# Optimization experiments

Hardware: AMD Instinct MI355X
Metric: run time of the kernel (lower is better)

The kernel has to match this reference:

```python
import jax, jax.numpy as jnp
import numpy as np

N = 50000      # nodes
E = 800000     # message-passing edges
EF = 1000000   # decoder (full) edges
IN = 128       # in_channels
H = 64         # hidden_channels
OUT = 1        # out_channels
T = 128        # num_timesteps
RESCALE = 4000.0  # SinusoidalPosEmb rescale_steps


def sinusoidal_pos_emb(t, dim, num_steps):
    # t: [N] int -> [N, dim]
    x = t.astype(jnp.float32) * (RESCALE / num_steps)
    half = dim // 2
    freqs = jnp.exp(jnp.arange(half, dtype=jnp.float32) * (-jnp.log(10000.0) / (half - 1)))
    ang = x[:, None] * freqs[None, :]            # [N, half]
    return jnp.concatenate([jnp.sin(ang), jnp.cos(ang)], axis=-1)


def gcn_conv(h, W, b, row, col, norm, n):
    # standard GCNConv: linear -> gather src -> scale by sym norm -> scatter-add to dst -> +bias
    x = h @ W                                     # [N, H]
    msg = x[row] * norm[:, None]                  # [E+N, H]
    out = jax.ops.segment_sum(msg, col, num_segments=n)
    return out + b


def setup_inputs() -> dict:
    key = jax.random.key(0)
    ks = jax.random.split(key, 12)
    rn = lambda k, shape, s=0.02: jax.random.normal(k, shape, jnp.float32) * s
    return {
        "x": jax.random.normal(ks[0], (N, IN), jnp.float32),
        "edge_index": jax.random.randint(ks[1], (2, E), 0, N, jnp.int32),
        "full_edge_index": jax.random.randint(ks[2], (2, EF), 0, N, jnp.int32),
        "time_steps": jax.random.randint(ks[3], (N,), 0, T, jnp.int32),
        "W_in": rn(ks[4], (IN, H)), "b_in": jnp.zeros((H,), jnp.float32),
        "W_t1": rn(ks[5], (H, 4 * H)), "b_t1": jnp.zeros((4 * H,), jnp.float32),
        "W_t2": rn(ks[6], (4 * H, H)), "b_t2": jnp.zeros((H,), jnp.float32),
        "W_c0": rn(ks[7], (H, H)), "b_c0": jnp.zeros((H,), jnp.float32),
        "W_c1": rn(ks[8], (H, H)), "b_c1": jnp.zeros((H,), jnp.float32),
        "W_d1": rn(ks[9], (2 * H, H)), "b_d1": jnp.zeros((H,), jnp.float32),
        "W_d2": rn(ks[10], (H, OUT)), "b_d2": jnp.zeros((OUT,), jnp.float32),
    }


def reference(x, edge_index, full_edge_index, time_steps,
              W_in, b_in, W_t1, b_t1, W_t2, b_t2,
              W_c0, b_c0, W_c1, b_c1, W_d1, b_d1, W_d2, b_d2):
    n = x.shape[0]
    # --- embedder (dropout is identity in eval mode) ---
    h = x @ W_in + b_in                                        # [N, H]
    pe = sinusoidal_pos_emb(time_steps, H, T)                  # [N, H]
    t_emb = jax.nn.silu(pe @ W_t1 + b_t1) @ W_t2 + b_t2        # [N, H]
    h_embed = h + t_emb

    # --- GCN encoder: add self-loops once, symmetric normalization ---
    loops = jnp.arange(n, dtype=edge_index.dtype)
    row = jnp.concatenate([edge_index[0], loops])              # [E+N]
    col = jnp.concatenate([edge_index[1], loops])
    deg = jax.ops.segment_sum(jnp.ones_like(col, jnp.float32), col, num_segments=n)
    dinv = jnp.where(deg > 0, jax.lax.rsqrt(deg), 0.0)
    norm = dinv[row] * dinv[col]                               # [E+N]

    h = gcn_conv(h_embed, W_c0, b_c0, row, col, norm, n)
    h = jax.nn.relu(h)                                         # act between layers; norm=None -> identity
    h_enc = gcn_conv(h, W_c1, b_c1, row, col, norm, n)

    # --- edge decoder: gather src/dst, concat, 2-layer SiLU MLP ---
    src, dst = full_edge_index[0], full_edge_index[1]
    feat = jnp.concatenate([h_enc[src], h_enc[dst]], axis=-1)  # [EF, 2H]
    edge_logits = jax.nn.silu(feat @ W_d1 + b_d1) @ W_d2 + b_d2  # [EF, OUT]
    return edge_logits, h_embed, h_enc
```

## Files before the change

kernel.cpp:

```cpp
#include <hip/hip_runtime.h>
#include <hip/hip_bf16.h>
#include <math.h>

#define N_NODES 50000
#define E_MSG   800000
#define E_FULL  1000000
#define IN_C    128
#define H_C     64
#define T_STEPS 128

#define OFF_Win   0
#define OFF_bin   8192
#define OFF_Wt1   8256
#define OFF_bt1   24640
#define OFF_Wt2   24896
#define OFF_bt2   41280
#define OFF_Wc0   41344
#define OFF_bc0   45440
#define OFF_Wc1   45504
#define OFF_bc1   49600
#define OFF_Wd1   49664
#define OFF_bd1   57856
#define OFF_Wd2   57920
#define OFF_bd2   57984
#define W_TOTAL   57985
#define OFF_BSUM  58016
#define OFF_BCUR  58272
#define OFF_FWD1  58624
#define OFF_FWIN  60672
#define OFF_FWC0  64768
#define OFF_TEMB  66816
#define OFF_DINV  75008
#define OFF_CNT   125008
#define OFF_PTR   175008
#define OFF_ELIST 225010
#define OFF_TMP2  1025012
#define OFF_ZBF   2625012
#define OFF_ZBF2  4225012
#define OFF_HENC8 5825012

#define OFF_FWC1  OFF_TMP2

#define SCAN_NB   ((N_NODES + 255) / 256)
#define BF_CH     ((E_MSG + SCAN_NB - 1) / SCAN_NB)
#define BC_NB     392
#define BC_CH     ((E_MSG + BC_NB - 1) / BC_NB)

typedef __attribute__((ext_vector_type(8))) short bf16x8;
typedef __attribute__((ext_vector_type(4))) float f32x4;

static __device__ __forceinline__ float bf2f(unsigned short u) {
    return __uint_as_float(((unsigned)u) << 16);
}
static __device__ __forceinline__ unsigned short f2bf(float f) {
    unsigned u = __float_as_uint(f);
    unsigned r = (u + 0x7fffu + ((u >> 16) & 1u)) >> 16;
    return (unsigned short)r;
}
static __device__ __forceinline__ unsigned char f2fp8(float f) {
    unsigned u = __float_as_uint(f);
    unsigned s = (u >> 24) & 0x80;
    float a = fminf(__uint_as_float(u & 0x7FFFFFFF), 448.0f);
    if (a < 0.015625f) {
        int qi = (int)rintf(a * 512.0f);
        return (unsigned char)(s | qi);
    }
    unsigned ua = __float_as_uint(a);
    int e = (int)((ua >> 23) & 0xFF) - 127;
    unsigned man = (ua & 0x7FFFFF) | 0x800000;
    unsigned r = man >> 20;
    unsigned rem = man & 0xFFFFF;
    if (rem > 0x80000u || (rem == 0x80000u && (r & 1))) r++;
    if (r == 16) { r = 8; e++; }
    if (e > 8) return (unsigned char)(s | 0x7E);
    return (unsigned char)(s | ((unsigned)(e + 7) << 3) | (r & 7));
}
static __device__ __forceinline__ bool detect_f32(const unsigned short* w, int* scnt) {
    if (threadIdx.x == 0) *scnt = 0;
    __syncthreads();
    int big = 0;
    for (int i = threadIdx.x; i < 2048; i += blockDim.x)
        if (fabsf(bf2f(w[2 * i])) > 0.5f) big++;
    atomicAdd(scnt, big);
    __syncthreads();
    return *scnt > 64;
}
static __device__ __forceinline__ float ldw(const void* p, int idx, bool f32) {
    return f32 ? ((const float*)p)[idx] : bf2f(((const unsigned short*)p)[idx]);
}

__global__ void __launch_bounds__(256) k_bcount(const int* __restrict__ col,
                                                int* __restrict__ bsum) {
    __shared__ int hist[SCAN_NB];
    int b = blockIdx.x, t = threadIdx.x;
    for (int i = t; i < SCAN_NB; i += 256) hist[i] = 0;
    __syncthreads();
    int lo = b * BC_CH;
    int hi = lo + BC_CH; if (hi > E_MSG) hi = E_MSG;
    for (int e = lo + t; e < hi; e += 256)
        atomicAdd(&hist[col[e] >> 8], 1);
    __syncthreads();
    for (int i = t; i < SCAN_NB; i += 256) {
        int c = hist[i];
        if (c > 0) atomicAdd(&bsum[i], c);
    }
}

__global__ void __launch_bounds__(256) k_scan2(int* __restrict__ bsum,
                                               int* __restrict__ bcur,
                                               int* __restrict__ ptr) {
    __shared__ int s[256];
    int t = threadIdx.x;
    int v = (t < SCAN_NB) ? bsum[t] : 0;
    s[t] = v;
    __syncthreads();
    for (int off = 1; off < 256; off <<= 1) {
        int u = (t >= off) ? s[t - off] : 0;
        __syncthreads();
        s[t] += u;
        __syncthreads();
    }
    if (t < SCAN_NB) { bsum[t] = s[t] - v; bcur[t] = s[t] - v; }
    if (t == 0) ptr[N_NODES] = E_MSG;
}

__global__ void __launch_bounds__(256) k_bfill(const int* __restrict__ row,
                                               const int* __restrict__ col,
                                               int* __restrict__ bcur,
                                               uint2* __restrict__ tmp) {
    __shared__ int hist[SCAN_NB];
    __shared__ int basew[SCAN_NB];
    int b = blockIdx.x;
    int lo = b * BF_CH;
    int hi = lo + BF_CH; if (hi > E_MSG) hi = E_MSG;
    for (int i = threadIdx.x; i < SCAN_NB; i += 256) hist[i] = 0;
    __syncthreads();
    for (int e = lo + threadIdx.x; e < hi; e += 256)
        atomicAdd(&hist[col[e] >> 8], 1);
    __syncthreads();
    for (int i = threadIdx.x; i < SCAN_NB; i += 256) {
        int c = hist[i];
        basew[i] = (c > 0) ? atomicAdd(&bcur[i], c) : 0;
    }
    __syncthreads();
    for (int i = threadIdx.x; i < SCAN_NB; i += 256) hist[i] = 0;
    __syncthreads();
    for (int e = lo + threadIdx.x; e < hi; e += 256) {
        int src = row[e], c = col[e];
        int bk = c >> 8;
        int off = atomicAdd(&hist[bk], 1);
        tmp[basew[bk] + off] = uint2{(unsigned)src, (unsigned)c};
    }
}

__global__ void __launch_bounds__(256) k_csort2(const uint2* __restrict__ tmp,
                                                const int* __restrict__ bsum,
                                                int* __restrict__ ptr,
                                                float* __restrict__ dinv,
                                                int* __restrict__ elist) {
    __shared__ int deg[256];
    __shared__ int pfx[256];
    int b = blockIdx.x, t = threadIdx.x;
    int start = bsum[b];
    int end = (b == SCAN_NB - 1) ? E_MSG : bsum[b + 1];

    deg[t] = 0;
    __syncthreads();
    for (int e = start + t; e < end; e += 256)
        atomicAdd(&deg[tmp[e].y & 255], 1);
    __syncthreads();

    int v = deg[t];
    pfx[t] = v;
    __syncthreads();
    for (int off = 1; off < 256; off <<= 1) {
        int u = (t >= off) ? pfx[t - off] : 0;
        __syncthreads();
        pfx[t] += u;
        __syncthreads();
    }
    int excl = pfx[t] - v;
    int n = (b << 8) + t;
    if (n < N_NODES) {
        ptr[n] = start + excl;
        dinv[n] = rsqrtf((float)v + 1.0f);
    }
    __syncthreads();
    deg[t] = excl;
    __syncthreads();
    for (int e = start + t; e < end; e += 256) {
        uint2 p = tmp[e];
        int pos = atomicAdd(&deg[p.y & 255], 1);
        elist[start + pos] = (int)p.x;
    }
}

#define WP_CVT_NB  227
#define WP_PREP_NB 96
#define WP_TEMB_NB 128

struct CvtArgs { const void* src[14]; };

__global__ void __launch_bounds__(256) k_wprep(CvtArgs a, float* ws) {
    __shared__ int scnt;
    bool f32 = detect_f32((const unsigned short*)a.src[0], &scnt);
    int bid = blockIdx.x;
    int tid = threadIdx.x;

    if (bid < WP_CVT_NB) {
        int t = bid * 256 + tid;
        if (t >= W_TOTAL) return;
        const int starts[14] = {OFF_Win, OFF_bin, OFF_Wt1, OFF_bt1, OFF_Wt2, OFF_bt2,
                                OFF_Wc0, OFF_bc0, OFF_Wc1, OFF_bc1, OFF_Wd1, OFF_bd1,
                                OFF_Wd2, OFF_bd2};
        int seg = 0;
#pragma unroll
        for (int i = 1; i < 14; i++)
            if (t >= starts[i]) seg = i;
        ws[t] = ldw(a.src[seg], t - starts[seg], f32);
    } else if (bid < WP_CVT_NB + WP_PREP_NB) {
        int idx = (bid - WP_CVT_NB) * 256 + tid;
        int local, j, lane, ct, c, t, m, q;
        if (idx < 8192) {
            local = idx;
            j = local & 7; lane = (local >> 3) & 63; ct = local >> 9;
            c = ct >> 2; t = ct & 3; m = lane & 15; q = lane >> 4;
            ((unsigned char*)(ws + OFF_FWD1))[local] =
                f2fp8(16.0f * ldw(a.src[10], (32 * c + 8 * q + j) * 64 + 16 * t + m, f32));
        } else if (idx < 16384) {
            local = idx - 8192;
            j = local & 7; lane = (local >> 3) & 63; ct = local >> 9;
            c = ct >> 2; t = ct & 3; m = lane & 15; q = lane >> 4;
            ((unsigned short*)(ws + OFF_FWIN))[local] =
                f2bf(ldw(a.src[0], (32 * c + 8 * q + j) * 64 + 16 * t + m, f32));
        } else if (idx < 20480) {
            local = idx - 16384;
            j = local & 7; lane = (local >> 3) & 63; ct = local >> 9;
            c = ct >> 2; t = ct & 3; m = lane & 15; q = lane >> 4;
            ((unsigned short*)(ws + OFF_FWC0))[local] =
                f2bf(ldw(a.src[6], (32 * c + 8 * q + j) * 64 + 16 * t + m, f32));
        } else {
            local = idx - 20480;
            j = local & 7; lane = (local >> 3) & 63; ct = local >> 9;
            c = ct >> 2; t = ct & 3; m = lane & 15; q = lane >> 4;
            ((unsigned short*)(ws + OFF_FWC1))[local] =
                f2bf(ldw(a.src[8], (32 * c + 8 * q + j) * 64 + 16 * t + m, f32));
        }
    } else {
        __shared__ float pe[64];
        __shared__ float us4[4][256];
        __shared__ float us[256];
        __shared__ float pcs[4][64];
        int j = tid & 63;
        int kg = tid >> 6;
        int t = bid - WP_CVT_NB - WP_PREP_NB;

        if (tid < 64) {
            float xt = (float)t * (4000.0f / 128.0f);
            float sc = -logf(10000.0f) / 31.0f;
            float fr = __expf((float)(tid & 31) * sc);
            float ang = xt * fr;
            pe[tid] = (tid < 32) ? sinf(ang) : cosf(ang);
        }
        __syncthreads();

        float pu[4] = {0.f, 0.f, 0.f, 0.f};
#pragma unroll
        for (int kk = 0; kk < 16; kk++) {
            int k = 16 * kg + kk;
            float p = pe[k];
#pragma unroll
            for (int q = 0; q < 4; q++)
                pu[q] = fmaf(p, ldw(a.src[2], k * 256 + q * 64 + j, f32), pu[q]);
        }
#pragma unroll
        for (int q = 0; q < 4; q++) us4[kg][q * 64 + j] = pu[q];
        __syncthreads();

        {
            float uu = ldw(a.src[3], tid, f32) +
                       us4[0][tid] + us4[1][tid] + us4[2][tid] + us4[3][tid];
            us[tid] = uu * __builtin_amdgcn_rcpf(1.0f + __expf(-uu));
        }
        __syncthreads();

        float pc = 0.f;
#pragma unroll
        for (int kk = 0; kk < 64; kk++) {
            int k = 64 * kg + kk;
            pc = fmaf(us[k], ldw(a.src[4], k * 64 + j, f32), pc);
        }
        pcs[kg][j] = pc;
        __syncthreads();
        if (tid < 64) {
            float acc = ldw(a.src[5], j, f32) +
                        pcs[0][j] + pcs[1][j] + pcs[2][j] + pcs[3][j];
            (ws + OFF_TEMB)[t * 64 + j] = acc;
        }
    }
}

__global__ void __launch_bounds__(256) k_embed(const void* __restrict__ xraw,
                                               const unsigned short* __restrict__ wdet,
                                               const int* __restrict__ tsteps,
                                               float* __restrict__ ws,
                                               float* __restrict__ out_hembed,
                                               unsigned short* __restrict__ zbf) {
    __shared__ int scnt;
    __shared__ unsigned short tl[4][16 * 64];
    bool f32 = detect_f32(wdet, &scnt);

    int lane = threadIdx.x & 63;
    int wv = threadIdx.x >> 6;
    int m = lane & 15, quad = lane >> 4;
    int wid = blockIdx.x * 4 + wv;
    if (wid > N_NODES / 16 - 1) wid = N_NODES / 16 - 1;
    int n0 = wid * 16;

    const unsigned short* fwin = (const unsigned short*)(ws + OFF_FWIN);
    const unsigned short* fwc0 = (const unsigned short*)(ws + OFF_FWC0);

    bf16x8 bI[4][4];
#pragma unroll
    for (int c = 0; c < 4; c++)
#pragma unroll
        for (int t = 0; t < 4; t++)
            bI[c][t] = *reinterpret_cast<const bf16x8*>(fwin + (c * 4 + t) * 512 + lane * 8);

    f32x4 acc[4] = {f32x4{0,0,0,0}, f32x4{0,0,0,0}, f32x4{0,0,0,0}, f32x4{0,0,0,0}};
#pragma unroll
    for (int c = 0; c < 4; c++) {
        bf16x8 a;
        if (f32) {
            const float* xp = (const float*)xraw + (size_t)(n0 + m) * 128 + 32 * c + 8 * quad;
            float4 v0 = *reinterpret_cast<const float4*>(xp);
            float4 v1 = *reinterpret_cast<const float4*>(xp + 4);
            a[0] = (short)f2bf(v0.x); a[1] = (short)f2bf(v0.y);
            a[2] = (short)f2bf(v0.z); a[3] = (short)f2bf(v0.w);
            a[4] = (short)f2bf(v1.x); a[5] = (short)f2bf(v1.y);
            a[6] = (short)f2bf(v1.z); a[7] = (short)f2bf(v1.w);
        } else {
            a = *reinterpret_cast<const bf16x8*>(
                (const unsigned short*)xraw + (size_t)(n0 + m) * 128 + 32 * c + 8 * quad);
        }
#pragma unroll
        for (int t = 0; t < 4; t++)
            acc[t] = __builtin_amdgcn_mfma_f32_16x16x32_bf16(a, bI[c][t], acc[t], 0, 0, 0);
    }

    int tn[4];
#pragma unroll
    for (int r = 0; r < 4; r++) tn[r] = tsteps[n0 + 4 * quad + r];
    const float* temb = ws + OFF_TEMB;
#pragma unroll
    for (int t = 0; t < 4; t++) {
        int ch = 16 * t + m;
        float bj = ws[OFF_bin + ch];
#pragma unroll
        for (int r = 0; r < 4; r++) {
            int node = n0 + 4 * quad + r;
            float v = acc[t][r] + bj + temb[tn[r] * 64 + ch];
            out_hembed[(size_t)node * 64 + ch] = v;
            tl[wv][(4 * quad + r) * 64 + ch] = f2bf(v);
        }
    }
    __syncthreads();

    bf16x8 bC[2][4];
#pragma unroll
    for (int c = 0; c < 2; c++)
#pragma unroll
        for (int t = 0; t < 4; t++)
            bC[c][t] = *reinterpret_cast<const bf16x8*>(fwc0 + (c * 4 + t) * 512 + lane * 8);

    f32x4 az[4] = {f32x4{0,0,0,0}, f32x4{0,0,0,0}, f32x4{0,0,0,0}, f32x4{0,0,0,0}};
#pragma unroll
    for (int c = 0; c < 2; c++) {
        bf16x8 a2 = *reinterpret_cast<const bf16x8*>(&tl[wv][m * 64 + 32 * c + 8 * quad]);
#pragma unroll
        for (int t = 0; t < 4; t++)
            az[t] = __builtin_amdgcn_mfma_f32_16x16x32_bf16(a2, bC[c][t], az[t], 0, 0, 0);
    }
    const float* dinv = ws + OFF_DINV;
    float dv[4];
#pragma unroll
    for (int r = 0; r < 4; r++) dv[r] = dinv[n0 + 4 * quad + r];
#pragma unroll
    for (int t = 0; t < 4; t++) {
        int ch = 16 * t + m;
#pragma unroll
        for (int r = 0; r < 4; r++)
            zbf[(size_t)(n0 + 4 * quad + r) * 64 + ch] = f2bf(az[t][r] * dv[r]);
    }
}

__global__ void __launch_bounds__(256) k_gather0(const unsigned short* __restrict__ zbf,
                                                 const int* __restrict__ ptr,
                                                 const int* __restrict__ elist,
                                                 const float* __restrict__ ws,
                                                 unsigned short* __restrict__ zout) {
    __shared__ unsigned short tile[16 * 64];
    const float* dinv = ws + OFF_DINV;
    const float* bias = ws + OFF_bc0;
    const unsigned short* fwc1 = (const unsigned short*)(ws + OFF_FWC1);

    int lane = threadIdx.x & 63;
    int wv = threadIdx.x >> 6;
    int g = lane >> 4;
    int cl = lane & 15;
    int n0 = blockIdx.x * 16;

    float4 b4 = *reinterpret_cast<const float4*>(bias + 4 * cl);

#pragma unroll
    for (int snode = 0; snode < 4; snode++) {
        int li = wv * 4 + snode;
        int n = n0 + li;
        int base = ptr[n], end = ptr[n + 1];

        float ws0 = (g == 0) ? 1.0f : 0.0f;
        ushort4 sv = *reinterpret_cast<const ushort4*>(zbf + (size_t)n * 64 + cl * 4);
        float s0 = ws0 * bf2f(sv.x), s1 = ws0 * bf2f(sv.y);
        float s2 = ws0 * bf2f(sv.z), s3 = ws0 * bf2f(sv.w);

        for (int k = base; k < end; k += 8) {
            int e0 = k + g, e1 = k + 4 + g;
            int r0 = elist[min(e0, end - 1)];
            int r1 = elist[min(e1, end - 1)];
            ushort4 v0 = *reinterpret_cast<const ushort4*>(zbf + (size_t)r0 * 64 + cl * 4);
            ushort4 v1 = *reinterpret_cast<const ushort4*>(zbf + (size_t)r1 * 64 + cl * 4);
            float w0 = (e0 < end) ? 1.0f : 0.0f;
            float w1 = (e1 < end) ? 1.0f : 0.0f;
            s0 = fmaf(w0, bf2f(v0.x), s0); s1 = fmaf(w0, bf2f(v0.y), s1);
            s2 = fmaf(w0, bf2f(v0.z), s2); s3 = fmaf(w0, bf2f(v0.w), s3);
            s0 = fmaf(w1, bf2f(v1.x), s0); s1 = fmaf(w1, bf2f(v1.y), s1);
            s2 = fmaf(w1, bf2f(v1.z), s2); s3 = fmaf(w1, bf2f(v1.w), s3);
        }
        s0 += __shfl_xor(s0, 16, 64); s0 += __shfl_xor(s0, 32, 64);
        s1 += __shfl_xor(s1, 16, 64); s1 += __shfl_xor(s1, 32, 64);
        s2 += __shfl_xor(s2, 16, 64); s2 += __shfl_xor(s2, 32, 64);
        s3 += __shfl_xor(s3, 16, 64); s3 += __shfl_xor(s3, 32, 64);

        if (g == 0) {
            float dv = dinv[n];
            float h0 = fmaxf(fmaf(dv, s0, b4.x), 0.0f);
            float h1 = fmaxf(fmaf(dv, s1, b4.y), 0.0f);
            float h2 = fmaxf(fmaf(dv, s2, b4.z), 0.0f);
            float h3 = fmaxf(fmaf(dv, s3, b4.w), 0.0f);
            ushort4 hv;
            hv.x = f2bf(h0); hv.y = f2bf(h1); hv.z = f2bf(h2); hv.w = f2bf(h3);
            int bo = li * 128 + ((cl * 8) ^ ((li & 7) << 4));
            *reinterpret_cast<ushort4*>((char*)tile + bo) = hv;
        }
    }
    __syncthreads();

    int m = lane & 15, q = lane >> 4;
    bf16x8 bB0 = *reinterpret_cast<const bf16x8*>(fwc1 + (0 * 4 + wv) * 512 + lane * 8);
    bf16x8 bB1 = *reinterpret_cast<const bf16x8*>(fwc1 + (1 * 4 + wv) * 512 + lane * 8);

    f32x4 az = f32x4{0, 0, 0, 0};
    {
        int bo0 = m * 128 + ((0 * 64 + q * 16) ^ ((m & 7) << 4));
        bf16x8 a0 = *reinterpret_cast<const bf16x8*>((const char*)tile + bo0);
        az = __builtin_amdgcn_mfma_f32_16x16x32_bf16(a0, bB0, az, 0, 0, 0);
        int bo1 = m * 128 + ((1 * 64 + q * 16) ^ ((m & 7) << 4));
        bf16x8 a1 = *reinterpret_cast<const bf16x8*>((const char*)tile + bo1);
        az = __builtin_amdgcn_mfma_f32_16x16x32_bf16(a1, bB1, az, 0, 0, 0);
    }
    float dv4[4];
#pragma unroll
    for (int r = 0; r < 4; r++) dv4[r] = dinv[n0 + 4 * q + r];
#pragma unroll
    for (int r = 0; r < 4; r++) {
        int node = n0 + 4 * q + r;
        zout[(size_t)node * 64 + 16 * wv + m] = f2bf(az[r] * dv4[r]);
    }
}

__global__ void __launch_bounds__(256) k_gather1(const unsigned short* __restrict__ zbf,
                                                 const int* __restrict__ ptr,
                                                 const int* __restrict__ elist,
                                                 const float* __restrict__ dinv,
                                                 const float* __restrict__ bias,
                                                 unsigned char* __restrict__ henc8,
                                                 float* __restrict__ ofp) {
    int lane = threadIdx.x & 63;
    int n = blockIdx.x * 4 + (threadIdx.x >> 6);
    int g = lane >> 4;
    int cl = lane & 15;
    int base = ptr[n], end = ptr[n + 1];

    float4 b4 = *reinterpret_cast<const float4*>(bias + 4 * cl);

    float ws0 = (g == 0) ? 1.0f : 0.0f;
    ushort4 sv = *reinterpret_cast<const ushort4*>(zbf + (size_t)n * 64 + cl * 4);
    float s0 = ws0 * bf2f(sv.x), s1 = ws0 * bf2f(sv.y);
    float s2 = ws0 * bf2f(sv.z), s3 = ws0 * bf2f(sv.w);

    for (int k = base; k < end; k += 8) {
        int e0 = k + g, e1 = k + 4 + g;
        int r0 = elist[min(e0, end - 1)];
        int r1 = elist[min(e1, end - 1)];
        ushort4 v0 = *reinterpret_cast<const ushort4*>(zbf + (size_t)r0 * 64 + cl * 4);
        ushort4 v1 = *reinterpret_cast<const ushort4*>(zbf + (size_t)r1 * 64 + cl * 4);
        float w0 = (e0 < end) ? 1.0f : 0.0f;
        float w1 = (e1 < end) ? 1.0f : 0.0f;
        s0 = fmaf(w0, bf2f(v0.x), s0); s1 = fmaf(w0, bf2f(v0.y), s1);
        s2 = fmaf(w0, bf2f(v0.z), s2); s3 = fmaf(w0, bf2f(v0.w), s3);
        s0 = fmaf(w1, bf2f(v1.x), s0); s1 = fmaf(w1, bf2f(v1.y), s1);
        s2 = fmaf(w1, bf2f(v1.z), s2); s3 = fmaf(w1, bf2f(v1.w), s3);
    }
    s0 += __shfl_xor(s0, 16, 64); s0 += __shfl_xor(s0, 32, 64);
    s1 += __shfl_xor(s1, 16, 64); s1 += __shfl_xor(s1, 32, 64);
    s2 += __shfl_xor(s2, 16, 64); s2 += __shfl_xor(s2, 32, 64);
    s3 += __shfl_xor(s3, 16, 64); s3 += __shfl_xor(s3, 32, 64);

    float dv = dinv[n];
    float o0 = fmaf(dv, s0, b4.x);
    float o1 = fmaf(dv, s1, b4.y);
    float o2 = fmaf(dv, s2, b4.z);
    float o3 = fmaf(dv, s3, b4.w);

    if (g == 0) {
        float4 ov; ov.x = o0; ov.y = o1; ov.z = o2; ov.w = o3;
        *reinterpret_cast<float4*>(ofp + (size_t)n * 64 + cl * 4) = ov;
    }
    int jc = lane >> 2;
    float a0 = __shfl(o0, jc, 64);
    float a1 = __shfl(o1, jc, 64);
    float a2 = __shfl(o2, jc, 64);
    float a3 = __shfl(o3, jc, 64);
    int sel = lane & 3;
    float mv = (sel == 0) ? a0 : (sel == 1) ? a1 : (sel == 2) ? a2 : a3;
    henc8[(size_t)n * 64 + lane] = f2fp8(16.0f * mv);
}

#define DEC_TPW 4
#define DEC_TILES (E_FULL / 16)

__global__ void __launch_bounds__(256) k_dec(const int* __restrict__ src,
                                             const int* __restrict__ dst,
                                             const unsigned char* __restrict__ h8,
                                             const float* __restrict__ ws,
                                             float* __restrict__ out) {
    int lane = threadIdx.x & 63;
    int wv = threadIdx.x >> 6;
    int m = lane & 15;
    int quad = lane >> 4;

    const unsigned char* fw = (const unsigned char*)(ws + OFF_FWD1);
    long bfr[4][4];
#pragma unroll
    for (int c = 0; c < 4; c++)
#pragma unroll
        for (int t = 0; t < 4; t++)
            bfr[c][t] = *reinterpret_cast<const long*>(fw + ((c * 4 + t) * 512 + lane * 8));

    float w2[4], b1v[4];
#pragma unroll
    for (int t = 0; t < 4; t++) {
        w2[t]  = ws[OFF_Wd2 + 16 * t + m];
        b1v[t] = ws[OFF_bd1 + 16 * t + m];
    }
    float b2 = ws[OFF_bd2];

    int tile0 = (blockIdx.x * 4 + wv) * DEC_TPW;
    int tc = min(tile0, DEC_TILES - 1);
    int s0 = src[tc * 16 + m], d0 = dst[tc * 16 + m];
    tc = min(tile0 + 1, DEC_TILES - 1);
    int s1 = src[tc * 16 + m], d1 = dst[tc * 16 + m];
    long A0[4];
#pragma unroll
    for (int c = 0; c < 4; c++) {
        int row = (c < 2) ? s0 : d0;
        A0[c] = *reinterpret_cast<const long*>(
            h8 + (size_t)row * 64 + (c & 1) * 32 + 8 * quad);
    }

    for (int i = 0; i < DEC_TPW; i++) {
        int tile = tile0 + i;
        int t2 = min(tile0 + i + 2, DEC_TILES - 1);
        int s2 = src[t2 * 16 + m], d2 = dst[t2 * 16 + m];
        long A1[4];
#pragma unroll
        for (int c = 0; c < 4; c++) {
            int row = (c < 2) ? s1 : d1;
            A1[c] = *reinterpret_cast<const long*>(
                h8 + (size_t)row * 64 + (c & 1) * 32 + 8 * quad);
        }
        f32x4 acc[4] = {f32x4{0,0,0,0}, f32x4{0,0,0,0}, f32x4{0,0,0,0}, f32x4{0,0,0,0}};
#pragma unroll
        for (int c = 0; c < 4; c++)
#pragma unroll
            for (int t = 0; t < 4; t++)
                acc[t] = __builtin_amdgcn_mfma_f32_16x16x32_fp8_fp8(A0[c], bfr[c][t], acc[t], 0, 0, 0);
        float sums[4];
#pragma unroll
        for (int r = 0; r < 4; r++) {
            float sv = 0.0f;
#pragma unroll
            for (int t = 0; t < 4; t++) {
                float v = fmaf(acc[t][r], 0.00390625f, b1v[t]);
                float h = v * __builtin_amdgcn_rcpf(1.0f + __expf(-v));
                sv = fmaf(h, w2[t], sv);
            }
#pragma unroll
            for (int msk = 8; msk >= 1; msk >>= 1)
                sv += __shfl_xor(sv, msk, 64);
            sums[r] = sv;
        }
        if (m == 0 && tile < DEC_TILES) {
            float4 o;
            o.x = sums[0] + b2; o.y = sums[1] + b2;
            o.z = sums[2] + b2; o.w = sums[3] + b2;
            *reinterpret_cast<float4*>(out + tile * 16 + 4 * quad) = o;
        }
#pragma unroll
        for (int c = 0; c < 4; c++) A0[c] = A1[c];
        s1 = s2; d1 = d2;
    }
}

extern "C" void kernel_launch(void* const* d_in, const int* in_sizes, int n_in,
                              void* d_out, int out_size, void* d_ws, size_t ws_size,
                              hipStream_t stream) {
    if (n_in < 18) return;
    const void* x              = d_in[0];
    const int* edge_index      = (const int*)d_in[1];
    const int* full_edge_index = (const int*)d_in[2];
    const int* tsteps          = (const int*)d_in[3];
    float* ws = (float*)d_ws;
    float* out = (float*)d_out;

    int*   iws   = (int*)d_ws;
    int*   bsum  = iws + OFF_BSUM;
    int*   bcur  = iws + OFF_BCUR;
    int*   ptr   = iws + OFF_PTR;
    int*   elist = iws + OFF_ELIST;
    uint2* tmp   = (uint2*)(iws + OFF_TMP2);
    unsigned short* zbf  = (unsigned short*)(ws + OFF_ZBF);
    unsigned short* zbf2 = (unsigned short*)(ws + OFF_ZBF2);
    unsigned char*  h8   = (unsigned char*)(ws + OFF_HENC8);

    CvtArgs ca;
    for (int i = 0; i < 14; i++) ca.src[i] = d_in[4 + i];

    hipMemsetAsync(bsum, 0, (size_t)SCAN_NB * 4, stream);
    k_bcount<<<BC_NB, 256, 0, stream>>>(edge_index + E_MSG, bsum);
    k_scan2<<<1, 256, 0, stream>>>(bsum, bcur, ptr);
    k_bfill<<<SCAN_NB, 256, 0, stream>>>(edge_index, edge_index + E_MSG, bcur, tmp);
    k_csort2<<<SCAN_NB, 256, 0, stream>>>(tmp, bsum, ptr, ws + OFF_DINV, elist);

    k_wprep<<<WP_CVT_NB + WP_PREP_NB + WP_TEMB_NB, 256, 0, stream>>>(ca, ws);

    k_embed<<<(N_NODES / 16 + 3) / 4, 256, 0, stream>>>(
        x, (const unsigned short*)d_in[4], tsteps, ws, out + E_FULL, zbf);

    k_gather0<<<N_NODES / 16, 256, 0, stream>>>(zbf, ptr, elist, ws, zbf2);

    k_gather1<<<N_NODES / 4, 256, 0, stream>>>(
        zbf2, ptr, elist, ws + OFF_DINV, ws + OFF_bc1, h8,
        out + E_FULL + (size_t)N_NODES * 64);

    int dec_blocks = (DEC_TILES + 4 * DEC_TPW - 1) / (4 * DEC_TPW);
    k_dec<<<dec_blocks, 256, 0, stream>>>(full_edge_index, full_edge_index + E_FULL,
                                          h8, ws, out);
}
```

Baseline: 263.3 us.

## Fuse bucket count into weight prep, drop scan kernel, transpose decoder MFMA reduction

The edge bucket-count pass is merged into the weight-prep launch, and the standalone single-block scan kernel is removed. In its place, both the fill and the sort kernels recompute the bucket prefix sum redundantly in shared memory, which saves two launches. The decoder MFMA operands are swapped so that each lane holds hidden units for one edge. That lets the epilogue reduce with two cross-lane shuffles instead of four per row, and store directly from lanes 0-15. FWC1 now gets its own workspace region rather than aliasing the temp buffer, since the temp buffer now overlaps in time with weight prep.

```diff
diff --git a/kernel.cpp b/kernel.cpp
--- a/kernel.cpp
+++ b/kernel.cpp
@@ -31,15 +31,13 @@
 #define OFF_FWC0  64768
 #define OFF_TEMB  66816
 #define OFF_DINV  75008
-#define OFF_CNT   125008
+#define OFF_FWC1  125008
 #define OFF_PTR   175008
 #define OFF_ELIST 225010
 #define OFF_TMP2  1025012
 #define OFF_ZBF   2625012
 #define OFF_ZBF2  4225012
 #define OFF_HENC8 5825012
-
-#define OFF_FWC1  OFF_TMP2
 
 #define SCAN_NB   ((N_NODES + 255) / 256)
 #define BF_CH     ((E_MSG + SCAN_NB - 1) / SCAN_NB)
@@ -89,63 +87,42 @@
     return f32 ? ((const float*)p)[idx] : bf2f(((const unsigned short*)p)[idx]);
 }
 
-__global__ void __launch_bounds__(256) k_bcount(const int* __restrict__ col,
-                                                int* __restrict__ bsum) {
+__global__ void __launch_bounds__(256) k_bfill(const int* __restrict__ row,
+                                               const int* __restrict__ col,
+                                               const int* __restrict__ btot,
+                                               int* __restrict__ bcur,
+                                               uint2* __restrict__ tmp) {
+    __shared__ int pref[256];
     __shared__ int hist[SCAN_NB];
+    __shared__ int basew[SCAN_NB];
     int b = blockIdx.x, t = threadIdx.x;
+
+    int tv = (t < SCAN_NB) ? btot[t] : 0;
+    pref[t] = tv;
+    __syncthreads();
+    for (int off = 1; off < 256; off <<= 1) {
+        int u = (t >= off) ? pref[t - off] : 0;
+        __syncthreads();
+        pref[t] += u;
+        __syncthreads();
+    }
+    int excl_t = pref[t] - tv;
+
+    int lo = b * BF_CH;
+    int hi = lo + BF_CH; if (hi > E_MSG) hi = E_MSG;
     for (int i = t; i < SCAN_NB; i += 256) hist[i] = 0;
     __syncthreads();
-    int lo = b * BC_CH;
-    int hi = lo + BC_CH; if (hi > E_MSG) hi = E_MSG;
     for (int e = lo + t; e < hi; e += 256)
         atomicAdd(&hist[col[e] >> 8], 1);
     __syncthreads();
-    for (int i = t; i < SCAN_NB; i += 256) {
-        int c = hist[i];
-        if (c > 0) atomicAdd(&bsum[i], c);
-    }
-}
-
-__global__ void __launch_bounds__(256) k_scan2(int* __restrict__ bsum,
-                                               int* __restrict__ bcur,
-                                               int* __restrict__ ptr) {
-    __shared__ int s[256];
-    int t = threadIdx.x;
-    int v = (t < SCAN_NB) ? bsum[t] : 0;
-    s[t] = v;
-    __syncthreads();
-    for (int off = 1; off < 256; off <<= 1) {
-        int u = (t >= off) ? s[t - off] : 0;
-        __syncthreads();
-        s[t] += u;
-        __syncthreads();
-    }
-    if (t < SCAN_NB) { bsum[t] = s[t] - v; bcur[t] = s[t] - v; }
-    if (t == 0) ptr[N_NODES] = E_MSG;
-}
-
-__global__ void __launch_bounds__(256) k_bfill(const int* __restrict__ row,
-                                               const int* __restrict__ col,
-                                               int* __restrict__ bcur,
-                                               uint2* __restrict__ tmp) {
-    __shared__ int hist[SCAN_NB];
-    __shared__ int basew[SCAN_NB];
-    int b = blockIdx.x;
-    int lo = b * BF_CH;
-    int hi = lo + BF_CH; if (hi > E_MSG) hi = E_MSG;
-    for (int i = threadIdx.x; i < SCAN_NB; i += 256) hist[i] = 0;
-    __syncthreads();
-    for (int e = lo + threadIdx.x; e < hi; e += 256)
-        atomicAdd(&hist[col[e] >> 8], 1);
-    __syncthreads();
-    for (int i = threadIdx.x; i < SCAN_NB; i += 256) {
-        int c = hist[i];
-        basew[i] = (c > 0) ? atomicAdd(&bcur[i], c) : 0;
-    }
-    __syncthreads();
-    for (int i = threadIdx.x; i < SCAN_NB; i += 256) hist[i] = 0;
-    __syncthreads();
-    for (int e = lo + threadIdx.x; e < hi; e += 256) {
+    if (t < SCAN_NB) {
+        int c = hist[t];
+        basew[t] = (c > 0) ? excl_t + atomicAdd(&bcur[t], c) : 0;
+    }
+    __syncthreads();
+    for (int i = t; i < SCAN_NB; i += 256) hist[i] = 0;
+    __syncthreads();
+    for (int e = lo + t; e < hi; e += 256) {
         int src = row[e], c = col[e];
         int bk = c >> 8;
         int off = atomicAdd(&hist[bk], 1);
@@ -154,15 +131,27 @@
 }
 
 __global__ void __launch_bounds__(256) k_csort2(const uint2* __restrict__ tmp,
-                                                const int* __restrict__ bsum,
+                                                const int* __restrict__ btot,
                                                 int* __restrict__ ptr,
                                                 float* __restrict__ dinv,
                                                 int* __restrict__ elist) {
     __shared__ int deg[256];
     __shared__ int pfx[256];
     int b = blockIdx.x, t = threadIdx.x;
-    int start = bsum[b];
-    int end = (b == SCAN_NB - 1) ? E_MSG : bsum[b + 1];
+
+    int tv = (t < SCAN_NB) ? btot[t] : 0;
+    pfx[t] = tv;
+    __syncthreads();
+    for (int off = 1; off < 256; off <<= 1) {
+        int u = (t >= off) ? pfx[t - off] : 0;
+        __syncthreads();
+        pfx[t] += u;
+        __syncthreads();
+    }
+    __shared__ int se[2];
+    if (t == b) { se[0] = pfx[t] - tv; se[1] = pfx[t]; }
+    __syncthreads();
+    int start = se[0], end = se[1];
 
     deg[t] = 0;
     __syncthreads();
@@ -185,6 +174,7 @@
         ptr[n] = start + excl;
         dinv[n] = rsqrtf((float)v + 1.0f);
     }
+    if (b == 0 && t == 0) ptr[N_NODES] = E_MSG;
     __syncthreads();
     deg[t] = excl;
     __syncthreads();
@@ -195,17 +185,40 @@
     }
 }
 
+#define WP_BC_NB   392
 #define WP_CVT_NB  227
 #define WP_PREP_NB 96
 #define WP_TEMB_NB 128
+#define WP_TOTAL_NB (WP_BC_NB + WP_CVT_NB + WP_PREP_NB + WP_TEMB_NB)
 
 struct CvtArgs { const void* src[14]; };
 
-__global__ void __launch_bounds__(256) k_wprep(CvtArgs a, float* ws) {
+__global__ void __launch_bounds__(256) k_wprep(CvtArgs a,
+                                               const int* __restrict__ ecol,
+                                               int* __restrict__ bsum,
+                                               float* ws) {
     __shared__ int scnt;
-    bool f32 = detect_f32((const unsigned short*)a.src[0], &scnt);
     int bid = blockIdx.x;
     int tid = threadIdx.x;
+
+    if (bid < WP_BC_NB) {
+        __shared__ int hist[SCAN_NB];
+        for (int i = tid; i < SCAN_NB; i += 256) hist[i] = 0;
+        __syncthreads();
+        int lo = bid * BC_CH;
+        int hi = lo + BC_CH; if (hi > E_MSG) hi = E_MSG;
+        for (int e = lo + tid; e < hi; e += 256)
+            atomicAdd(&hist[ecol[e] >> 8], 1);
+        __syncthreads();
+        for (int i = tid; i < SCAN_NB; i += 256) {
+            int c = hist[i];
+            if (c > 0) atomicAdd(&bsum[i], c);
+        }
+        return;
+    }
+    bid -= WP_BC_NB;
+
+    bool f32 = detect_f32((const unsigned short*)a.src[0], &scnt);
 
     if (bid < WP_CVT_NB) {
         int t = bid * 256 + tid;
@@ -557,11 +570,11 @@
         for (int t = 0; t < 4; t++)
             bfr[c][t] = *reinterpret_cast<const long*>(fw + ((c * 4 + t) * 512 + lane * 8));
 
-    float w2[4], b1v[4];
-#pragma unroll
-    for (int t = 0; t < 4; t++) {
-        w2[t]  = ws[OFF_Wd2 + 16 * t + m];
-        b1v[t] = ws[OFF_bd1 + 16 * t + m];
+    float4 w2v[4], b1v[4];
+#pragma unroll
+    for (int mt = 0; mt < 4; mt++) {
+        w2v[mt] = *reinterpret_cast<const float4*>(ws + OFF_Wd2 + 16 * mt + 4 * quad);
+        b1v[mt] = *reinterpret_cast<const float4*>(ws + OFF_bd1 + 16 * mt + 4 * quad);
     }
     float b2 = ws[OFF_bd2];
 
@@ -593,29 +606,27 @@
 #pragma unroll
         for (int c = 0; c < 4; c++)
 #pragma unroll
-            for (int t = 0; t < 4; t++)
-                acc[t] = __builtin_amdgcn_mfma_f32_16x16x32_fp8_fp8(A0[c], bfr[c][t], acc[t], 0, 0, 0);
-        float sums[4];
-#pragma unroll
-        for (int r = 0; r < 4; r++) {
-            float sv = 0.0f;
-#pragma unroll
-            for (int t = 0; t < 4; t++) {
-                float v = fmaf(acc[t][r], 0.00390625f, b1v[t]);
+            for (int mt = 0; mt < 4; mt++)
+                acc[mt] = __builtin_amdgcn_mfma_f32_16x16x32_fp8_fp8(bfr[c][mt], A0[c], acc[mt], 0, 0, 0);
+
+        float p[4];
+#pragma unroll
+        for (int mt = 0; mt < 4; mt++) {
+            float pm = 0.0f;
+#pragma unroll
+            for (int r = 0; r < 4; r++) {
+                float v = fmaf(acc[mt][r], 0.00390625f, b1v[mt][r]);
                 float h = v * __builtin_amdgcn_rcpf(1.0f + __expf(-v));
-                sv = fmaf(h, w2[t], sv);
+                pm = fmaf(h, w2v[mt][r], pm);
             }
-#pragma unroll
-            for (int msk = 8; msk >= 1; msk >>= 1)
-                sv += __shfl_xor(sv, msk, 64);
-            sums[r] = sv;
-        }
-        if (m == 0 && tile < DEC_TILES) {
-            float4 o;
-            o.x = sums[0] + b2; o.y = sums[1] + b2;
-            o.z = sums[2] + b2; o.w = sums[3] + b2;
-            *reinterpret_cast<float4*>(out + tile * 16 + 4 * quad) = o;
-        }
+            p[mt] = pm;
+        }
+        float sv = (p[0] + p[1]) + (p[2] + p[3]);
+        sv += __shfl_xor(sv, 16, 64);
+        sv += __shfl_xor(sv, 32, 64);
+        if (lane < 16 && tile < DEC_TILES)
+            out[tile * 16 + lane] = sv + b2;
+
 #pragma unroll
         for (int c = 0; c < 4; c++) A0[c] = A1[c];
         s1 = s2; d1 = d2;
@@ -646,13 +657,13 @@
     CvtArgs ca;
     for (int i = 0; i < 14; i++) ca.src[i] = d_in[4 + i];
 
-    hipMemsetAsync(bsum, 0, (size_t)SCAN_NB * 4, stream);
-    k_bcount<<<BC_NB, 256, 0, stream>>>(edge_index + E_MSG, bsum);
-    k_scan2<<<1, 256, 0, stream>>>(bsum, bcur, ptr);
-    k_bfill<<<SCAN_NB, 256, 0, stream>>>(edge_index, edge_index + E_MSG, bcur, tmp);
+    hipMemsetAsync(bsum, 0, (size_t)512 * 4, stream);
+
+    k_wprep<<<WP_TOTAL_NB, 256, 0, stream>>>(ca, edge_index + E_MSG, bsum, ws);
+
+    k_bfill<<<SCAN_NB, 256, 0, stream>>>(edge_index, edge_index + E_MSG, bsum,
+                                         bcur, tmp);
     k_csort2<<<SCAN_NB, 256, 0, stream>>>(tmp, bsum, ptr, ws + OFF_DINV, elist);
-
-    k_wprep<<<WP_CVT_NB + WP_PREP_NB + WP_TEMB_NB, 256, 0, stream>>>(ca, ws);
 
     k_embed<<<(N_NODES / 16 + 3) / 4, 256, 0, stream>>>(
         x, (const unsigned short*)d_in[4], tsteps, ws, out + E_FULL, zbf);
```

New measurement: 262.7 us. No clear change (-0.2%).
